# Performance work log

Hardware: AMD Instinct MI355X
Metric: run time of the kernel (lower is better)

Reference implementation:

```python
import jax, jax.numpy as jnp
import numpy as np

EMB = 8
HID = 64
B = 1000
T = 512
N = (B * T) // 5  # events per source; sources partition the (batch,time) grid

_KEYS = ["ccba", "cdtx", "cust", "dp", "remit"]
_NUMS = {"ccba": 8, "cdtx": 1, "cust": 1, "dp": 2, "remit": 1}
_CATS = {"ccba": 0, "cdtx": 2, "cust": 3, "dp": 8, "remit": 1}
_VOCAB = {"ccba": 0, "cdtx": 179, "cust": 37, "dp": 435, "remit": 5}


def setup_inputs() -> dict:
    ks = iter(jax.random.split(jax.random.key(0), 64))
    rng = np.random.default_rng(0)
    chunks = np.split(rng.permutation(B * T), 5)
    d = {}
    for k5, ch in zip(_KEYS, chunks):
        d[k5 + "_num"] = jax.random.normal(next(ks), (N, _NUMS[k5]), jnp.float32)
        if _CATS[k5] > 0:
            d[k5 + "_cat"] = jax.random.randint(next(ks), (N, _CATS[k5]), 0, _VOCAB[k5])
            d[k5 + "_tab"] = jax.random.normal(next(ks), (_VOCAB[k5], EMB), jnp.float32) * 0.1
        d[k5 + "_bi"] = jnp.asarray(ch // T, jnp.int32)
        d[k5 + "_ti"] = jnp.asarray(ch % T, jnp.int32)
        in_dim = _CATS[k5] * EMB + _NUMS[k5]
        d[k5 + "_W"] = jax.random.normal(next(ks), (in_dim, HID), jnp.float32) * np.float32(1.0 / np.sqrt(in_dim))
        d[k5 + "_b"] = jnp.zeros((HID,), jnp.float32)
    # LSTM: 2 layers x 2 directions, hidden 64, proj_size 1 -> layer1 input is 2
    for l, insz in [(0, HID), (1, 2)]:
        d[f"Wih{l}"] = jax.random.normal(next(ks), (2, 4 * HID, insz), jnp.float32) * 0.05
        d[f"Whh{l}"] = jax.random.normal(next(ks), (2, 4 * HID, 1), jnp.float32) * 0.05
        d[f"Whr{l}"] = jax.random.normal(next(ks), (2, 1, HID), jnp.float32) * 0.05
        d[f"bih{l}"] = jnp.zeros((2, 4 * HID), jnp.float32)
        d[f"bhh{l}"] = jnp.zeros((2, 4 * HID), jnp.float32)
    d["length"] = T
    d["batch_size"] = B
    return d


def _embed(num, cat, tab, W, b):
    # FeatureEmbedder: concat(categorical embeddings, numeric) -> Linear(hidden)
    x = num if cat is None else jnp.concatenate([tab[cat].reshape(cat.shape[0], -1), num], axis=-1)
    return x @ W + b


def _lstm_dir(x, Wih, Whh, Whr, bih, bhh, reverse):
    Bx = x.shape[0]
    H = Whr.shape[1]
    p = Whr.shape[0]
    bias = bih + bhh

    def step(carry, xt):
        h, c = carry  # h: [B,p] projected hidden, c: [B,H] cell
        g = xt @ Wih.T + h @ Whh.T + bias
        i, f, gg, o = jnp.split(g, 4, axis=-1)  # PyTorch gate order i,f,g,o
        c = jax.nn.sigmoid(f) * c + jax.nn.sigmoid(i) * jnp.tanh(gg)
        h = (jax.nn.sigmoid(o) * jnp.tanh(c)) @ Whr.T  # proj_size projection
        return (h, c), h

    init = (jnp.zeros((Bx, p), x.dtype), jnp.zeros((Bx, H), x.dtype))
    _, ys = jax.lax.scan(step, init, jnp.swapaxes(x, 0, 1), reverse=reverse)
    return jnp.swapaxes(ys, 0, 1)  # [B,T,p]


def _bilstm(x, Wih, Whh, Whr, bih, bhh):
    fwd = _lstm_dir(x, Wih[0], Whh[0], Whr[0], bih[0], bhh[0], False)
    bwd = _lstm_dir(x, Wih[1], Whh[1], Whr[1], bih[1], bhh[1], True)
    return jnp.concatenate([fwd, bwd], axis=-1)


def _forward(a):
    feat = jnp.zeros((a["batch_size"], a["length"], HID), jnp.float32)
    for k5 in _KEYS:
        v = _embed(a[k5 + "_num"], a.get(k5 + "_cat"), a.get(k5 + "_tab"), a[k5 + "_W"], a[k5 + "_b"])
        feat = feat.at[a[k5 + "_bi"], a[k5 + "_ti"]].set(v)  # scatter-assemble padded tensor
    h = _bilstm(feat, a["Wih0"], a["Whh0"], a["Whr0"], a["bih0"], a["bhh0"])
    h = _bilstm(h, a["Wih1"], a["Whh1"], a["Whr1"], a["bih1"], a["bhh1"])
    return h.mean(axis=2)  # [B,T]


def reference(ccba_num, ccba_bi, ccba_ti, ccba_W, ccba_b,
              cdtx_num, cdtx_cat, cdtx_tab, cdtx_bi, cdtx_ti, cdtx_W, cdtx_b,
              cust_num, cust_cat, cust_tab, cust_bi, cust_ti, cust_W, cust_b,
              dp_num, dp_cat, dp_tab, dp_bi, dp_ti, dp_W, dp_b,
              remit_num, remit_cat, remit_tab, remit_bi, remit_ti, remit_W, remit_b,
              Wih0, Whh0, Whr0, bih0, bhh0, Wih1, Whh1, Whr1, bih1, bhh1,
              length, batch_size):
    return _forward(dict(locals()))
```

## Files before the change

### kernel.cpp

```cpp
#include <hip/hip_runtime.h>
#include <cstdint>
#include <cstddef>

#define TLEN 512
#define BATCH 1000
#define NEVS 102400
#define HID 64
#define W0S 8
#define NP (TLEN / W0S)

__device__ __forceinline__ float fast_rcp(float x) {
#if __has_builtin(__builtin_amdgcn_rcpf)
    return __builtin_amdgcn_rcpf(x);
#else
    return 1.0f / x;
#endif
}
__device__ __forceinline__ float sigm(float x) { return fast_rcp(1.0f + __expf(-x)); }
__device__ __forceinline__ float tanh_f(float x) { return fmaf(2.0f, sigm(2.0f * x), -1.0f); }

__device__ __forceinline__ float wave_sum_bcast(float x) {
#if __has_builtin(__builtin_amdgcn_update_dpp) && __has_builtin(__builtin_amdgcn_readlane)
    x += __int_as_float(__builtin_amdgcn_update_dpp(0, __float_as_int(x), 0x111, 0xf, 0xf, true));
    x += __int_as_float(__builtin_amdgcn_update_dpp(0, __float_as_int(x), 0x112, 0xf, 0xf, true));
    x += __int_as_float(__builtin_amdgcn_update_dpp(0, __float_as_int(x), 0x114, 0xf, 0xf, true));
    x += __int_as_float(__builtin_amdgcn_update_dpp(0, __float_as_int(x), 0x118, 0xf, 0xf, true));
    x += __int_as_float(__builtin_amdgcn_update_dpp(0, __float_as_int(x), 0x142, 0xa, 0xf, true));
    x += __int_as_float(__builtin_amdgcn_update_dpp(0, __float_as_int(x), 0x143, 0xc, 0xf, true));
    return __int_as_float(__builtin_amdgcn_readlane(__float_as_int(x), 63));
#else
#pragma unroll
    for (int off = 1; off < 64; off <<= 1) x += __shfl_xor(x, off, 64);
    return x;
#endif
}

__device__ __forceinline__ void wave_sum2(float& a, float& b) {
#if __has_builtin(__builtin_amdgcn_update_dpp) && __has_builtin(__builtin_amdgcn_readlane)
    int ta, tb;
    ta = __builtin_amdgcn_update_dpp(0, __float_as_int(a), 0x111, 0xf, 0xf, true);
    tb = __builtin_amdgcn_update_dpp(0, __float_as_int(b), 0x111, 0xf, 0xf, true);
    a += __int_as_float(ta); b += __int_as_float(tb);
    ta = __builtin_amdgcn_update_dpp(0, __float_as_int(a), 0x112, 0xf, 0xf, true);
    tb = __builtin_amdgcn_update_dpp(0, __float_as_int(b), 0x112, 0xf, 0xf, true);
    a += __int_as_float(ta); b += __int_as_float(tb);
    ta = __builtin_amdgcn_update_dpp(0, __float_as_int(a), 0x114, 0xf, 0xf, true);
    tb = __builtin_amdgcn_update_dpp(0, __float_as_int(b), 0x114, 0xf, 0xf, true);
    a += __int_as_float(ta); b += __int_as_float(tb);
    ta = __builtin_amdgcn_update_dpp(0, __float_as_int(a), 0x118, 0xf, 0xf, true);
    tb = __builtin_amdgcn_update_dpp(0, __float_as_int(b), 0x118, 0xf, 0xf, true);
    a += __int_as_float(ta); b += __int_as_float(tb);
    ta = __builtin_amdgcn_update_dpp(0, __float_as_int(a), 0x142, 0xa, 0xf, true);
    tb = __builtin_amdgcn_update_dpp(0, __float_as_int(b), 0x142, 0xa, 0xf, true);
    a += __int_as_float(ta); b += __int_as_float(tb);
    ta = __builtin_amdgcn_update_dpp(0, __float_as_int(a), 0x143, 0xc, 0xf, true);
    tb = __builtin_amdgcn_update_dpp(0, __float_as_int(b), 0x143, 0xc, 0xf, true);
    a += __int_as_float(ta); b += __int_as_float(tb);
    a = __int_as_float(__builtin_amdgcn_readlane(__float_as_int(a), 63));
    b = __int_as_float(__builtin_amdgcn_readlane(__float_as_int(b), 63));
#else
    a = wave_sum_bcast(a); b = wave_sum_bcast(b);
#endif
}

__global__ __launch_bounds__(256) void map_build_kernel(
    const int* __restrict__ b0, const int* __restrict__ t0,
    const int* __restrict__ b1, const int* __restrict__ t1,
    const int* __restrict__ b2, const int* __restrict__ t2,
    const int* __restrict__ b3, const int* __restrict__ t3,
    const int* __restrict__ b4, const int* __restrict__ t4,
    int* __restrict__ map)
{
    const int src = blockIdx.y;
    const int* bi = src == 0 ? b0 : src == 1 ? b1 : src == 2 ? b2 : src == 3 ? b3 : b4;
    const int* ti = src == 0 ? t0 : src == 1 ? t1 : src == 2 ? t2 : src == 3 ? t3 : t4;
    const int e = blockIdx.x * 256 + threadIdx.x;
    map[bi[e] * TLEN + ti[e]] = (src << 20) | e;
}

__global__ __launch_bounds__(512) void compose_kernel(
    const float* __restrict__ W0, const float* __restrict__ B0,
    const float* __restrict__ W1, const float* __restrict__ B1,
    const float* __restrict__ W2, const float* __restrict__ B2,
    const float* __restrict__ W3, const float* __restrict__ B3,
    const float* __restrict__ W4, const float* __restrict__ B4,
    const float* __restrict__ Wih, const float* __restrict__ bih,
    const float* __restrict__ bhh, float* __restrict__ wp)
{
    const int col = threadIdx.x;
    const int row = blockIdx.x;
    const float* srcW; const float* srcB; int base, IND;
    if (row < 9)        { srcW = W0; srcB = B0; base = 0;   IND = 8;  }
    else if (row < 27)  { srcW = W1; srcB = B1; base = 9;   IND = 17; }
    else if (row < 53)  { srcW = W2; srcB = B2; base = 27;  IND = 25; }
    else if (row < 120) { srcW = W3; srcB = B3; base = 53;  IND = 66; }
    else                { srcW = W4; srcB = B4; base = 120; IND = 9;  }
    const int j = row - base;
    const float* xrow = (j < IND) ? (srcW + (size_t)j * 64) : srcB;
    const float* wr = Wih + (size_t)col * 64;
    float acc = 0.0f;
#pragma unroll
    for (int h2 = 0; h2 < 64; ++h2) acc = fmaf(xrow[h2], wr[h2], acc);
    if (j == IND) acc += bih[col] + bhh[col];
    wp[(size_t)row * 512 + col] = acc;
}

template<int NB, int BASE>
__device__ __forceinline__ float4 dot4(const float* wT, const float* xb, int colq) {
    float ax = 0.f, ay = 0.f, az = 0.f, aw = 0.f;
#pragma unroll
    for (int jb = 0; jb < NB; ++jb) {
        const float4 x4 = *(const float4*)(xb + 4 * jb);
        const float* w = wT + (size_t)(BASE + 4 * jb) * 256 + 4 * colq;
        const float4 w0 = *(const float4*)(w);
        const float4 w1 = *(const float4*)(w + 256);
        const float4 w2 = *(const float4*)(w + 512);
        const float4 w3 = *(const float4*)(w + 768);
        ax = fmaf(x4.x, w0.x, ax); ay = fmaf(x4.x, w0.y, ay);
        az = fmaf(x4.x, w0.z, az); aw = fmaf(x4.x, w0.w, aw);
        ax = fmaf(x4.y, w1.x, ax); ay = fmaf(x4.y, w1.y, ay);
        az = fmaf(x4.y, w1.z, az); aw = fmaf(x4.y, w1.w, aw);
        ax = fmaf(x4.z, w2.x, ax); ay = fmaf(x4.z, w2.y, ay);
        az = fmaf(x4.z, w2.z, az); aw = fmaf(x4.z, w2.w, aw);
        ax = fmaf(x4.w, w3.x, ax); ay = fmaf(x4.w, w3.y, ay);
        az = fmaf(x4.w, w3.z, az); aw = fmaf(x4.w, w3.w, aw);
    }
    return make_float4(ax, ay, az, aw);
}

__global__ __launch_bounds__(576, 1) void fused0_kernel(
    const float* __restrict__ ccba_num,
    const float* __restrict__ cdtx_num, const int* __restrict__ cdtx_cat, const float* __restrict__ cdtx_tab,
    const float* __restrict__ cust_num, const int* __restrict__ cust_cat, const float* __restrict__ cust_tab,
    const float* __restrict__ dp_num,   const int* __restrict__ dp_cat,   const float* __restrict__ dp_tab,
    const float* __restrict__ remit_num, const int* __restrict__ remit_cat, const float* __restrict__ remit_tab,
    const float* __restrict__ wp, const int* __restrict__ map,
    const float* __restrict__ Whh, const float* __restrict__ Whr,
    float* __restrict__ h0)
{
    __shared__ float wT[132 * 256];
    __shared__ float winP[2][W0S][256];
    __shared__ float xbuf[2][W0S][68];
    __shared__ int   mcls[2][W0S];

    const int tid = threadIdx.x;
    const int b = blockIdx.x >> 1, dir = blockIdx.x & 1;

    {
        const float4* wp4 = (const float4*)wp;
        float4* wT4 = (float4*)wT;
        for (int i = tid; i < 130 * 64; i += 576) {
            const int row = i >> 6, c4 = i & 63;
            wT4[(row << 6) + c4] = wp4[(row << 7) + (dir << 6) + c4];
        }
        if (tid < 128) wT4[130 * 64 + tid] = make_float4(0.f, 0.f, 0.f, 0.f);
    }

    float whh4[4] = {0.f, 0.f, 0.f, 0.f};
    float whr = 0.f, h = 0.f, c = 0.f;
    float* h0p = h0 + (size_t)b * TLEN * 2 + dir;
    if (tid >= 512) {
        const int lane = tid - 512;
#pragma unroll
        for (int k = 0; k < 4; ++k) whh4[k] = Whh[dir * 256 + k * 64 + lane];
        whr = Whr[dir * HID + lane];
    }

    struct GR { float v0, v1; int mc; };

    auto g_load = [&](int P) -> GR {
        GR g; g.v0 = 0.f; g.v1 = 0.f;
        const int ev = tid >> 6, v = tid & 63;
        const int s = P * W0S + ev;
        const int t = dir ? (TLEN - 1 - s) : s;
        g.mc = map[b * TLEN + t];
        const int src = g.mc >> 20, e = g.mc & 0xFFFFF;
        switch (src) {
        case 0:
            g.v0 = (v < 8) ? ccba_num[(size_t)e * 8 + v] : (v == 8 ? 1.0f : 0.0f);
            break;
        case 1:
            g.v0 = (v < 16) ? cdtx_tab[(size_t)cdtx_cat[e * 2 + (v >> 3)] * 8 + (v & 7)]
                 : (v == 16 ? cdtx_num[e] : (v == 17 ? 1.0f : 0.0f));
            break;
        case 2:
            g.v0 = (v < 24) ? cust_tab[(size_t)cust_cat[e * 3 + (v >> 3)] * 8 + (v & 7)]
                 : (v == 24 ? cust_num[e] : (v == 25 ? 1.0f : 0.0f));
            break;
        case 3:
            g.v0 = dp_tab[(size_t)dp_cat[e * 8 + (v >> 3)] * 8 + (v & 7)];
            if (v < 4) g.v1 = (v < 2) ? dp_num[(size_t)e * 2 + v] : (v == 2 ? 1.0f : 0.0f);
            break;
        default:
            g.v0 = (v < 8) ? remit_tab[(size_t)remit_cat[e] * 8 + v]
                 : (v == 8 ? remit_num[e] : (v == 9 ? 1.0f : 0.0f));
            break;
        }
        return g;
    };
    auto g_store = [&](const GR& g, int P) {
        const int buf = P & 1;
        const int ev = tid >> 6, v = tid & 63;
        if (v == 0) mcls[buf][ev] = g.mc;
        const int src = g.mc >> 20;
        const int pad = (src == 0) ? 12 : (src == 1) ? 20 : (src == 2) ? 28
                      : (src == 3) ? 64 : 12;
        if (v < pad) xbuf[buf][ev][v] = g.v0;
        if (src == 3 && v < 4) xbuf[buf][ev][64 + v] = g.v1;
    };

    auto a1 = [&](int P) {
        const int buf = P & 1;
        const int ev = tid >> 6, colq = tid & 63;
        const int src = mcls[buf][ev] >> 20;
        const float* xb = xbuf[buf][ev];
        float4 acc;
        switch (src) {
        case 0:  acc = dot4<3, 0>(wT, xb, colq);   break;
        case 1:  acc = dot4<5, 9>(wT, xb, colq);   break;
        case 2:  acc = dot4<7, 27>(wT, xb, colq);  break;
        case 3:  acc = dot4<17, 53>(wT, xb, colq); break;
        default: acc = dot4<3, 120>(wT, xb, colq); break;
        }
        ((float4*)winP[buf][ev])[colq] = acc;
    };

    auto bstep = [&](int P) {
        const int buf = P & 1;
        const int lane = tid - 512;
        for (int sl = 0; sl < W0S; ++sl) {
            const float gi = fmaf(whh4[0], h, winP[buf][sl][lane]);
            const float gf = fmaf(whh4[1], h, winP[buf][sl][64 + lane]);
            const float gg = fmaf(whh4[2], h, winP[buf][sl][128 + lane]);
            const float go = fmaf(whh4[3], h, winP[buf][sl][192 + lane]);
            c = sigm(gf) * c + sigm(gi) * tanh_f(gg);
            h = wave_sum_bcast(sigm(go) * tanh_f(c) * whr);
            const int s = P * W0S + sl;
            const int tt = dir ? (TLEN - 1 - s) : s;
            if (lane == 0) h0p[(size_t)tt * 2] = h;
        }
    };

    if (tid < 512) { GR g0 = g_load(0); g_store(g0, 0); }
    __syncthreads();
    if (tid < 512) { GR g1 = g_load(1); a1(0); g_store(g1, 1); }
    __syncthreads();

    for (int p = 0; p < NP; ++p) {
        if (tid < 512) {
            GR g{};
            const bool hg = (p + 2 < NP);
            if (hg) g = g_load(p + 2);
            if (p + 1 < NP) a1(p + 1);
            if (hg) g_store(g, p + 2);
        } else if (tid < 576) {
            bstep(p);
        }
        __syncthreads();
    }
}

__global__ __launch_bounds__(256, 2) void lstm1_kernel(
    const float* __restrict__ h0, const float* __restrict__ Wih,
    const float* __restrict__ Whh, const float* __restrict__ Whr,
    const float* __restrict__ bih, const float* __restrict__ bhh,
    float* __restrict__ h1)
{
    __shared__ float2 xsh[4][TLEN];
    const int w = threadIdx.x >> 6, lane = threadIdx.x & 63;
    const int b0 = blockIdx.x * 4;
    const int b = b0 + w;

    {
        const float2* src = (const float2*)(h0 + (size_t)b0 * TLEN * 2);
        for (int i = threadIdx.x; i < 4 * TLEN; i += 256)
            xsh[i >> 9][i & 511] = src[i];
    }

    const volatile float* vWih = Wih;
    const volatile float* vWhh = Whh;
    const volatile float* vWhr = Whr;
    const volatile float* vbih = bih;
    const volatile float* vbhh = bhh;

    float wi0[2][4], wi1[2][4], whh[2][4], bias[2][4], whr[2];
#pragma unroll
    for (int d = 0; d < 2; ++d) {
#pragma unroll
        for (int k = 0; k < 4; ++k) {
            const int r = d * 256 + k * 64 + lane;
            wi0[d][k] = vWih[(size_t)r * 2 + 0];
            wi1[d][k] = vWih[(size_t)r * 2 + 1];
            whh[d][k] = vWhh[r];
            bias[d][k] = vbih[r] + vbhh[r];
        }
        whr[d] = vWhr[d * HID + lane];
    }
    __syncthreads();

    float hA = 0, cA = 0, hB = 0, cB = 0;
    const float2* hb = xsh[w];

    float2 xA = hb[0];
    float2 xB = hb[TLEN - 1];
    for (int t = 0; t < TLEN; ++t) {
        const int tn = (t + 1 < TLEN) ? t + 1 : t;
        const float2 xAn = hb[tn];
        const float2 xBn = hb[TLEN - 1 - tn];
        float gA[4], gB[4];
#pragma unroll
        for (int k = 0; k < 4; ++k) {
            gA[k] = fmaf(whh[0][k], hA, fmaf(wi1[0][k], xA.y, fmaf(wi0[0][k], xA.x, bias[0][k])));
            gB[k] = fmaf(whh[1][k], hB, fmaf(wi1[1][k], xB.y, fmaf(wi0[1][k], xB.x, bias[1][k])));
        }
        cA = sigm(gA[1]) * cA + sigm(gA[0]) * tanh_f(gA[2]);
        cB = sigm(gB[1]) * cB + sigm(gB[0]) * tanh_f(gB[2]);
        float pA = sigm(gA[3]) * tanh_f(cA) * whr[0];
        float pB = sigm(gB[3]) * tanh_f(cB) * whr[1];
        wave_sum2(pA, pB);
        hA = pA; hB = pB;
        if (lane == 0) {
            h1[((size_t)b * TLEN + t) * 2 + 0] = hA;
            h1[((size_t)b * TLEN + (TLEN - 1 - t)) * 2 + 1] = hB;
        }
        xA = xAn; xB = xBn;
    }
}

__global__ __launch_bounds__(256) void mean_kernel(
    const float2* __restrict__ h1, float* __restrict__ out)
{
    int i = blockIdx.x * 256 + threadIdx.x;
    if (i < BATCH * TLEN) {
        float2 v = h1[i];
        out[i] = 0.5f * (v.x + v.y);
    }
}

extern "C" void kernel_launch(void* const* d_in, const int* in_sizes, int n_in,
                              void* d_out, int out_size, void* d_ws, size_t ws_size,
                              hipStream_t stream)
{
    const float* ccba_num = (const float*)d_in[0];
    const int*   ccba_bi  = (const int*)d_in[1];
    const int*   ccba_ti  = (const int*)d_in[2];
    const float* ccba_W   = (const float*)d_in[3];
    const float* ccba_b   = (const float*)d_in[4];
    const float* cdtx_num = (const float*)d_in[5];
    const int*   cdtx_cat = (const int*)d_in[6];
    const float* cdtx_tab = (const float*)d_in[7];
    const int*   cdtx_bi  = (const int*)d_in[8];
    const int*   cdtx_ti  = (const int*)d_in[9];
    const float* cdtx_W   = (const float*)d_in[10];
    const float* cdtx_b   = (const float*)d_in[11];
    const float* cust_num = (const float*)d_in[12];
    const int*   cust_cat = (const int*)d_in[13];
    const float* cust_tab = (const float*)d_in[14];
    const int*   cust_bi  = (const int*)d_in[15];
    const int*   cust_ti  = (const int*)d_in[16];
    const float* cust_W   = (const float*)d_in[17];
    const float* cust_b   = (const float*)d_in[18];
    const float* dp_num   = (const float*)d_in[19];
    const int*   dp_cat   = (const int*)d_in[20];
    const float* dp_tab   = (const float*)d_in[21];
    const int*   dp_bi    = (const int*)d_in[22];
    const int*   dp_ti    = (const int*)d_in[23];
    const float* dp_W     = (const float*)d_in[24];
    const float* dp_b     = (const float*)d_in[25];
    const float* remit_num = (const float*)d_in[26];
    const int*   remit_cat = (const int*)d_in[27];
    const float* remit_tab = (const float*)d_in[28];
    const int*   remit_bi  = (const int*)d_in[29];
    const int*   remit_ti  = (const int*)d_in[30];
    const float* remit_W   = (const float*)d_in[31];
    const float* remit_b   = (const float*)d_in[32];
    const float* Wih0 = (const float*)d_in[33];
    const float* Whh0 = (const float*)d_in[34];
    const float* Whr0 = (const float*)d_in[35];
    const float* bih0 = (const float*)d_in[36];
    const float* bhh0 = (const float*)d_in[37];
    const float* Wih1 = (const float*)d_in[38];
    const float* Whh1 = (const float*)d_in[39];
    const float* Whr1 = (const float*)d_in[40];
    const float* bih1 = (const float*)d_in[41];
    const float* bhh1 = (const float*)d_in[42];

    float* out = (float*)d_out;

    char* ws = (char*)d_ws;
    float* wp  = (float*)ws;
    int*   map = (int*)  (ws + 266240ull);
    float* h0  = (float*)(ws + 266240ull + 2048000ull);
    float* h1  = (float*)(ws + 266240ull + 2048000ull + 4096000ull);

    compose_kernel<<<130, 512, 0, stream>>>(
        ccba_W, ccba_b, cdtx_W, cdtx_b, cust_W, cust_b,
        dp_W, dp_b, remit_W, remit_b, Wih0, bih0, bhh0, wp);

    map_build_kernel<<<dim3(NEVS / 256, 5), 256, 0, stream>>>(
        ccba_bi, ccba_ti, cdtx_bi, cdtx_ti, cust_bi, cust_ti,
        dp_bi, dp_ti, remit_bi, remit_ti, map);

    fused0_kernel<<<2 * BATCH, 576, 0, stream>>>(
        ccba_num,
        cdtx_num, cdtx_cat, cdtx_tab,
        cust_num, cust_cat, cust_tab,
        dp_num, dp_cat, dp_tab,
        remit_num, remit_cat, remit_tab,
        wp, map, Whh0, Whr0, h0);

    lstm1_kernel<<<250, 256, 0, stream>>>(h0, Wih1, Whh1, Whr1, bih1, bhh1, h1);
    mean_kernel<<<(BATCH * TLEN + 255) / 256, 256, 0, stream>>>((const float2*)h1, out);
}
```

Baseline: 1.426 ms.

## Split fused layer-0 LSTM into chunked projection and recurrence kernels

Replaces the fused kernel, where eight waves projected inputs while one wave ran the recurrence per (batch, direction) block, with two kernels launched alternately over time chunks. A projection kernel writes the gate pre-activations for a chunk of timesteps to a global workspace, and a lightweight recurrence kernel runs four (batch, direction) sequences per 256-thread block, carrying h and c across chunks through global buffers. This frees the recurrence from the one-block-per-CU occupancy limit of the fused kernel and lets many serial chains run concurrently. In exchange it adds global memory traffic for the gates, many kernel launches, and a chunk size that depends on workspace size.

```diff
diff --git a/kernel.cpp b/kernel.cpp
--- a/kernel.cpp
+++ b/kernel.cpp
@@ -6,8 +6,6 @@
 #define BATCH 1000
 #define NEVS 102400
 #define HID 64
-#define W0S 8
-#define NP (TLEN / W0S)
 
 __device__ __forceinline__ float fast_rcp(float x) {
 #if __has_builtin(__builtin_amdgcn_rcpf)
@@ -128,136 +126,157 @@
     return make_float4(ax, ay, az, aw);
 }
 
-__global__ __launch_bounds__(576, 1) void fused0_kernel(
+__global__ __launch_bounds__(512, 1) void project_kernel(
     const float* __restrict__ ccba_num,
     const float* __restrict__ cdtx_num, const int* __restrict__ cdtx_cat, const float* __restrict__ cdtx_tab,
     const float* __restrict__ cust_num, const int* __restrict__ cust_cat, const float* __restrict__ cust_tab,
     const float* __restrict__ dp_num,   const int* __restrict__ dp_cat,   const float* __restrict__ dp_tab,
     const float* __restrict__ remit_num, const int* __restrict__ remit_cat, const float* __restrict__ remit_tab,
     const float* __restrict__ wp, const int* __restrict__ map,
-    const float* __restrict__ Whh, const float* __restrict__ Whr,
-    float* __restrict__ h0)
+    float* __restrict__ gf, float* __restrict__ gb,
+    int f0, int len, int tcm)
 {
     __shared__ float wT[132 * 256];
-    __shared__ float winP[2][W0S][256];
-    __shared__ float xbuf[2][W0S][68];
-    __shared__ int   mcls[2][W0S];
+    __shared__ float xbuf[8][2][68];
 
     const int tid = threadIdx.x;
-    const int b = blockIdx.x >> 1, dir = blockIdx.x & 1;
+    const int wv = tid >> 6, lane = tid & 63;
+    const int bg = blockIdx.x, dir = blockIdx.y;
+    float* gdst = dir ? gb : gf;
 
     {
         const float4* wp4 = (const float4*)wp;
         float4* wT4 = (float4*)wT;
-        for (int i = tid; i < 130 * 64; i += 576) {
+        for (int i = tid; i < 130 * 64; i += 512) {
             const int row = i >> 6, c4 = i & 63;
             wT4[(row << 6) + c4] = wp4[(row << 7) + (dir << 6) + c4];
         }
         if (tid < 128) wT4[130 * 64 + tid] = make_float4(0.f, 0.f, 0.f, 0.f);
     }
-
-    float whh4[4] = {0.f, 0.f, 0.f, 0.f};
-    float whr = 0.f, h = 0.f, c = 0.f;
-    float* h0p = h0 + (size_t)b * TLEN * 2 + dir;
-    if (tid >= 512) {
-        const int lane = tid - 512;
-#pragma unroll
-        for (int k = 0; k < 4; ++k) whh4[k] = Whh[dir * 256 + k * 64 + lane];
-        whr = Whr[dir * HID + lane];
-    }
-
-    struct GR { float v0, v1; int mc; };
-
-    auto g_load = [&](int P) -> GR {
-        GR g; g.v0 = 0.f; g.v1 = 0.f;
-        const int ev = tid >> 6, v = tid & 63;
-        const int s = P * W0S + ev;
-        const int t = dir ? (TLEN - 1 - s) : s;
+    __syncthreads();
+
+    struct GX { float x0, x1; int mc; };
+
+    auto g_load = [&](int bl, int lt) -> GX {
+        GX g; g.x0 = 0.f; g.x1 = 0.f;
+        const int b = bg * 4 + bl;
+        const int t = dir ? (TLEN - 1 - f0 - lt) : (f0 + lt);
         g.mc = map[b * TLEN + t];
         const int src = g.mc >> 20, e = g.mc & 0xFFFFF;
+        const int v = lane;
         switch (src) {
         case 0:
-            g.v0 = (v < 8) ? ccba_num[(size_t)e * 8 + v] : (v == 8 ? 1.0f : 0.0f);
+            if (v < 8) g.x0 = ccba_num[(size_t)e * 8 + v];
+            else if (v == 8) g.x0 = 1.0f;
             break;
         case 1:
-            g.v0 = (v < 16) ? cdtx_tab[(size_t)cdtx_cat[e * 2 + (v >> 3)] * 8 + (v & 7)]
-                 : (v == 16 ? cdtx_num[e] : (v == 17 ? 1.0f : 0.0f));
+            if (v < 16) g.x0 = cdtx_tab[(size_t)cdtx_cat[e * 2 + (v >> 3)] * 8 + (v & 7)];
+            else if (v == 16) g.x0 = cdtx_num[e];
+            else if (v == 17) g.x0 = 1.0f;
             break;
         case 2:
-            g.v0 = (v < 24) ? cust_tab[(size_t)cust_cat[e * 3 + (v >> 3)] * 8 + (v & 7)]
-                 : (v == 24 ? cust_num[e] : (v == 25 ? 1.0f : 0.0f));
+            if (v < 24) g.x0 = cust_tab[(size_t)cust_cat[e * 3 + (v >> 3)] * 8 + (v & 7)];
+            else if (v == 24) g.x0 = cust_num[e];
+            else if (v == 25) g.x0 = 1.0f;
             break;
         case 3:
-            g.v0 = dp_tab[(size_t)dp_cat[e * 8 + (v >> 3)] * 8 + (v & 7)];
-            if (v < 4) g.v1 = (v < 2) ? dp_num[(size_t)e * 2 + v] : (v == 2 ? 1.0f : 0.0f);
+            g.x0 = dp_tab[(size_t)dp_cat[e * 8 + (v >> 3)] * 8 + (v & 7)];
+            if (v < 2) g.x1 = dp_num[(size_t)e * 2 + v];
+            else if (v == 2) g.x1 = 1.0f;
             break;
         default:
-            g.v0 = (v < 8) ? remit_tab[(size_t)remit_cat[e] * 8 + v]
-                 : (v == 8 ? remit_num[e] : (v == 9 ? 1.0f : 0.0f));
+            if (v < 8) g.x0 = remit_tab[(size_t)remit_cat[e] * 8 + v];
+            else if (v == 8) g.x0 = remit_num[e];
+            else if (v == 9) g.x0 = 1.0f;
             break;
         }
         return g;
     };
-    auto g_store = [&](const GR& g, int P) {
-        const int buf = P & 1;
-        const int ev = tid >> 6, v = tid & 63;
-        if (v == 0) mcls[buf][ev] = g.mc;
-        const int src = g.mc >> 20;
-        const int pad = (src == 0) ? 12 : (src == 1) ? 20 : (src == 2) ? 28
-                      : (src == 3) ? 64 : 12;
-        if (v < pad) xbuf[buf][ev][v] = g.v0;
-        if (src == 3 && v < 4) xbuf[buf][ev][64 + v] = g.v1;
-    };
-
-    auto a1 = [&](int P) {
-        const int buf = P & 1;
-        const int ev = tid >> 6, colq = tid & 63;
-        const int src = mcls[buf][ev] >> 20;
-        const float* xb = xbuf[buf][ev];
+
+    int bl = 0, lt = wv, buf = 0;
+    GX cur = g_load(bl, lt);
+    while (bl < 4) {
+        int nbl = bl, nlt = lt + 8;
+        if (nlt >= len) { nbl = bl + 1; nlt = wv; }
+
+        xbuf[wv][buf][lane] = cur.x0;
+        if (lane < 4) xbuf[wv][buf][64 + lane] = cur.x1;
+
+        GX nxt{};
+        if (nbl < 4) nxt = g_load(nbl, nlt);
+
+        const int src = __builtin_amdgcn_readfirstlane(cur.mc) >> 20;
+        const float* xb = xbuf[wv][buf];
         float4 acc;
         switch (src) {
-        case 0:  acc = dot4<3, 0>(wT, xb, colq);   break;
-        case 1:  acc = dot4<5, 9>(wT, xb, colq);   break;
-        case 2:  acc = dot4<7, 27>(wT, xb, colq);  break;
-        case 3:  acc = dot4<17, 53>(wT, xb, colq); break;
-        default: acc = dot4<3, 120>(wT, xb, colq); break;
-        }
-        ((float4*)winP[buf][ev])[colq] = acc;
+        case 0:  acc = dot4<3, 0>(wT, xb, lane);   break;
+        case 1:  acc = dot4<5, 9>(wT, xb, lane);   break;
+        case 2:  acc = dot4<7, 27>(wT, xb, lane);  break;
+        case 3:  acc = dot4<17, 53>(wT, xb, lane); break;
+        default: acc = dot4<3, 120>(wT, xb, lane); break;
+        }
+        const int b = bg * 4 + bl;
+        *(float4*)&gdst[((size_t)(b * tcm + lt)) * 256 + 4 * lane] = acc;
+
+        bl = nbl; lt = nlt; cur = nxt; buf ^= 1;
+    }
+}
+
+__global__ __launch_bounds__(256) void rec_chunk_kernel(
+    const float* __restrict__ gf, const float* __restrict__ gb,
+    const float* __restrict__ Whh, const float* __restrict__ Whr,
+    float* __restrict__ h0, float* __restrict__ hs, float* __restrict__ cs,
+    int f0, int len, int tcm, int first)
+{
+    const int wv = threadIdx.x >> 6, lane = threadIdx.x & 63;
+    const int p = blockIdx.x * 4 + wv;
+    const int b = p >> 1, dir = p & 1;
+
+    float whh4[4];
+#pragma unroll
+    for (int k = 0; k < 4; ++k) whh4[k] = Whh[dir * 256 + k * 64 + lane];
+    const float whr = Whr[dir * HID + lane];
+
+    const float* g = (dir ? gb : gf) + (size_t)b * tcm * 256 + lane;
+    float* h0p = h0 + (size_t)b * TLEN * 2 + dir;
+
+    float h, c;
+    if (first) { h = 0.0f; c = 0.0f; }
+    else       { h = hs[p]; c = cs[(size_t)p * 64 + lane]; }
+
+    auto ga = [&](int s) -> const float* {
+        const int sc = (s < len) ? s : (len - 1);
+        return g + (size_t)sc * 256;
     };
-
-    auto bstep = [&](int P) {
-        const int buf = P & 1;
-        const int lane = tid - 512;
-        for (int sl = 0; sl < W0S; ++sl) {
-            const float gi = fmaf(whh4[0], h, winP[buf][sl][lane]);
-            const float gf = fmaf(whh4[1], h, winP[buf][sl][64 + lane]);
-            const float gg = fmaf(whh4[2], h, winP[buf][sl][128 + lane]);
-            const float go = fmaf(whh4[3], h, winP[buf][sl][192 + lane]);
-            c = sigm(gf) * c + sigm(gi) * tanh_f(gg);
-            h = wave_sum_bcast(sigm(go) * tanh_f(c) * whr);
-            const int s = P * W0S + sl;
-            const int tt = dir ? (TLEN - 1 - s) : s;
-            if (lane == 0) h0p[(size_t)tt * 2] = h;
-        }
+    auto do_step = [&](const float (&G)[4], int s) {
+        const float gi = fmaf(whh4[0], h, G[0]);
+        const float gfv = fmaf(whh4[1], h, G[1]);
+        const float gg = fmaf(whh4[2], h, G[2]);
+        const float go = fmaf(whh4[3], h, G[3]);
+        c = sigm(gfv) * c + sigm(gi) * tanh_f(gg);
+        h = wave_sum_bcast(sigm(go) * tanh_f(c) * whr);
+        const int t_out = dir ? (TLEN - 1 - f0 - s) : (f0 + s);
+        if (lane == 0) h0p[(size_t)t_out * 2] = h;
     };
 
-    if (tid < 512) { GR g0 = g_load(0); g_store(g0, 0); }
-    __syncthreads();
-    if (tid < 512) { GR g1 = g_load(1); a1(0); g_store(g1, 1); }
-    __syncthreads();
-
-    for (int p = 0; p < NP; ++p) {
-        if (tid < 512) {
-            GR g{};
-            const bool hg = (p + 2 < NP);
-            if (hg) g = g_load(p + 2);
-            if (p + 1 < NP) a1(p + 1);
-            if (hg) g_store(g, p + 2);
-        } else if (tid < 576) {
-            bstep(p);
-        }
-        __syncthreads();
-    }
+    float A[4], B[4];
+    {
+        const float* pa = ga(0); const float* pb = ga(1);
+#pragma unroll
+        for (int k = 0; k < 4; ++k) { A[k] = pa[k * 64]; B[k] = pb[k * 64]; }
+    }
+    for (int s = 0; s < len; s += 2) {
+        float C[4], D[4];
+        const float* pc = ga(s + 2); const float* pd = ga(s + 3);
+#pragma unroll
+        for (int k = 0; k < 4; ++k) { C[k] = pc[k * 64]; D[k] = pd[k * 64]; }
+        do_step(A, s);
+        if (s + 1 < len) do_step(B, s + 1);
+#pragma unroll
+        for (int k = 0; k < 4; ++k) { A[k] = C[k]; B[k] = D[k]; }
+    }
+    if (lane == 0) hs[p] = h;
+    cs[(size_t)p * 64 + lane] = c;
 }
 
 __global__ __launch_bounds__(256, 2) void lstm1_kernel(
@@ -387,11 +406,25 @@
 
     float* out = (float*)d_out;
 
+    const size_t FIXED = 4096000ull + 4096000ull + 266240ull + 8000ull
+                       + 512000ull + 2048000ull;
+    size_t avail = (ws_size > FIXED) ? (ws_size - FIXED) : 0;
+    int tcm = (int)(avail / 2048000ull);
+    if (tcm < 1) tcm = 1;
+    if (tcm > 86) tcm = 86;
+    if (tcm >= 2) tcm &= ~1;
+
     char* ws = (char*)d_ws;
-    float* wp  = (float*)ws;
-    int*   map = (int*)  (ws + 266240ull);
-    float* h0  = (float*)(ws + 266240ull + 2048000ull);
-    float* h1  = (float*)(ws + 266240ull + 2048000ull + 4096000ull);
+    const size_t gfB = (size_t)tcm * 1024000ull;
+    float* gf    = (float*)ws;
+    float* gb    = (float*)(ws + gfB);
+    char*  fixed = ws + 2 * gfB;
+    float* h0    = (float*)fixed;
+    float* h1    = (float*)(fixed + 4096000ull);
+    float* wp    = (float*)(fixed + 8192000ull);
+    float* hs    = (float*)(fixed + 8192000ull + 266240ull);
+    float* cs    = (float*)(fixed + 8192000ull + 266240ull + 8000ull);
+    int*   map   = (int*)  (fixed + 8192000ull + 266240ull + 8000ull + 512000ull);
 
     compose_kernel<<<130, 512, 0, stream>>>(
         ccba_W, ccba_b, cdtx_W, cdtx_b, cust_W, cust_b,
@@ -401,13 +434,20 @@
         ccba_bi, ccba_ti, cdtx_bi, cdtx_ti, cust_bi, cust_ti,
         dp_bi, dp_ti, remit_bi, remit_ti, map);
 
-    fused0_kernel<<<2 * BATCH, 576, 0, stream>>>(
-        ccba_num,
-        cdtx_num, cdtx_cat, cdtx_tab,
-        cust_num, cust_cat, cust_tab,
-        dp_num, dp_cat, dp_tab,
-        remit_num, remit_cat, remit_tab,
-        wp, map, Whh0, Whr0, h0);
+    int first = 1;
+    for (int f0 = 0; f0 < TLEN; f0 += tcm) {
+        const int len = (TLEN - f0 < tcm) ? (TLEN - f0) : tcm;
+        project_kernel<<<dim3(250, 2), 512, 0, stream>>>(
+            ccba_num,
+            cdtx_num, cdtx_cat, cdtx_tab,
+            cust_num, cust_cat, cust_tab,
+            dp_num, dp_cat, dp_tab,
+            remit_num, remit_cat, remit_tab,
+            wp, map, gf, gb, f0, len, tcm);
+        rec_chunk_kernel<<<500, 256, 0, stream>>>(
+            gf, gb, Whh0, Whr0, h0, hs, cs, f0, len, tcm, first);
+        first = 0;
+    }
 
     lstm1_kernel<<<250, 256, 0, stream>>>(h0, Wih1, Whh1, Whr1, bih1, bhh1, h1);
     mean_kernel<<<(BATCH * TLEN + 255) / 256, 256, 0, stream>>>((const float2*)h1, out);
```

Measured after the change: 1.316 ms. -7.7%, faster.
